# Kernel optimization log

Measured on AMD Instinct MI355X. Metric: run time of the kernel, lower is better.

## Reference

```python
import jax, jax.numpy as jnp
import numpy as np

N, E, H, DE = 50000, 800000, 128, 16

def silu(x):
    return x * jax.nn.sigmoid(x)

def setup_inputs() -> dict:
    key = jax.random.key(0)
    ks = jax.random.split(key, 24)
    def W(k, i, o, s=0.02):
        return (jax.random.normal(k, (i, o), jnp.float32) * s)
    inp = {
        'h': jax.random.normal(ks[0], (N, H), jnp.float32),
        'coord': jax.random.normal(ks[1], (N, 3), jnp.float32),
        'edge_index': jax.random.randint(ks[2], (2, E), 0, N),
        'edge_attr': jax.random.normal(ks[3], (E, DE), jnp.float32),
        # mes_mlp: Linear(2H+1+DE -> H), SiLU, Linear(H -> H), SiLU
        'mes_w1': W(ks[4], 2 * H + 1 + DE, H), 'mes_b1': jnp.zeros((H,), jnp.float32),
        'mes_w2': W(ks[5], H, H),              'mes_b2': jnp.zeros((H,), jnp.float32),
        # edge_mlp: Linear(H+1+DE -> H), SiLU, Linear(H -> H)
        'edge_w1': W(ks[6], H + 1 + DE, H),    'edge_b1': jnp.zeros((H,), jnp.float32),
        'edge_w2': W(ks[7], H, H),             'edge_b2': jnp.zeros((H,), jnp.float32),
        # node_mlp: Linear(H+H -> H), SiLU, Linear(H -> H)
        'node_w1': W(ks[8], 2 * H, H),         'node_b1': jnp.zeros((H,), jnp.float32),
        'node_w2': W(ks[9], H, H),             'node_b2': jnp.zeros((H,), jnp.float32),
        # coord_mlp: Linear(H -> H), SiLU, Linear(H -> 1, no bias, xavier gain 0.001)
        'coord_w1': W(ks[10], H, H),           'coord_b1': jnp.zeros((H,), jnp.float32),
        'coord_w2': W(ks[11], H, 1, s=0.001),
    }
    return inp

def reference(h, coord, edge_index, edge_attr,
              mes_w1, mes_b1, mes_w2, mes_b2,
              edge_w1, edge_b1, edge_w2, edge_b2,
              node_w1, node_b1, node_w2, node_b2,
              coord_w1, coord_b1, coord_w2):
    row, col = edge_index[0], edge_index[1]
    n = h.shape[0]
    # coord2radial
    coord_diff = coord[row] - coord[col]                        # [E,3]
    radial = jnp.sum(coord_diff ** 2, axis=1, keepdims=True)    # [E,1]
    norm = jnp.sqrt(radial + 1e-8)
    coord_diff = coord_diff / (norm + 1.0)
    # mes_model
    mes_in = jnp.concatenate([h[row], h[col], radial, edge_attr], axis=1)
    edge_feat = silu(silu(mes_in @ mes_w1 + mes_b1) @ mes_w2 + mes_b2)  # [E,H]
    # coord_model (agg='sum', no tanh)
    trans = coord_diff * (silu(edge_feat @ coord_w1 + coord_b1) @ coord_w2)  # [E,3]
    coord = coord + jax.ops.segment_sum(trans, col, num_segments=n)
    # node_model (recurrent)
    agg = jax.ops.segment_sum(edge_feat, col, num_segments=n)   # [N,H]
    node_in = jnp.concatenate([h, agg], axis=1)
    h = h + (silu(node_in @ node_w1 + node_b1) @ node_w2 + node_b2)
    # edge_model
    edge_in = jnp.concatenate([edge_feat, radial, edge_attr], axis=1)
    edge_out = silu(edge_in @ edge_w1 + edge_b1) @ edge_w2 + edge_b2
    return (h, coord, edge_out)
```

## Files before the change

kernel.cpp:

```cpp
#include <hip/hip_runtime.h>
#include <cstdint>
#include <cstddef>

typedef float f32x4 __attribute__((ext_vector_type(4)));
typedef __bf16 bf16x8 __attribute__((ext_vector_type(8)));
typedef __bf16 bf16x4 __attribute__((ext_vector_type(4)));
typedef unsigned short u16;

#define Hdim 128
#define DEdim 16
#define TP 40

__device__ __forceinline__ float bf2f(uint32_t lo16){
  return __builtin_bit_cast(float, lo16 << 16);
}
__device__ __forceinline__ float bfhi(uint32_t v){
  return __builtin_bit_cast(float, v & 0xffff0000u);
}
__device__ __forceinline__ float silu_f(float x){
  return x * __builtin_amdgcn_rcpf(1.0f + __expf(-x));
}
__device__ __forceinline__ uint2 pack4(f32x4 v){
  bf16x4 p;
  #pragma unroll
  for (int i=0;i<4;++i) p[i] = (__bf16)v[i];
  return __builtin_bit_cast(uint2, p);
}
__device__ __forceinline__ uint2 silu_pack4(const f32x4& v, f32x4* sout=nullptr){
  f32x4 s;
  #pragma unroll
  for (int i=0;i<4;++i) s[i] = silu_f(v[i]);
  if (sout) *sout = s;
  return pack4(s);
}

template<int KC>
__device__ __forceinline__ void gemm_sw(
    const u16* A, int apitch,
    const u16* __restrict__ Wt, int kpad, int woff,
    int wv, int cidx, int hi, f32x4 (&acc)[4][2])
{
  const u16* w0p = Wt + (size_t)((wv*2+0)*16 + cidx)*kpad + woff + hi*8;
  const u16* w1p = Wt + (size_t)((wv*2+1)*16 + cidx)*kpad + woff + hi*8;
  const u16* ap  = A + (size_t)cidx*apitch + hi*8;
  #pragma unroll
  for (int kc=0; kc<KC; ++kc){
    bf16x8 w0 = *(const bf16x8*)(w0p + kc*32);
    bf16x8 w1 = *(const bf16x8*)(w1p + kc*32);
    #pragma unroll
    for (int et=0; et<4; ++et){
      bf16x8 a = *(const bf16x8*)(ap + et*16*apitch + kc*32);
      acc[et][0] = __builtin_amdgcn_mfma_f32_16x16x32_bf16(w0, a, acc[et][0], 0,0,0);
      acc[et][1] = __builtin_amdgcn_mfma_f32_16x16x32_bf16(w1, a, acc[et][1], 0,0,0);
    }
  }
}

__device__ __forceinline__ void acc_bias(const float* __restrict__ bias,
                                         int wv, int hi, f32x4 (&acc)[4][2])
{
  f32x4 b0 = *(const f32x4*)(bias + (wv*2+0)*16 + hi*4);
  f32x4 b1 = *(const f32x4*)(bias + (wv*2+1)*16 + hi*4);
  #pragma unroll
  for (int et=0;et<4;++et){ acc[et][0]=b0; acc[et][1]=b1; }
}

template<int SP>
__device__ __forceinline__ void write_silu_S(u16* S, f32x4 (&acc)[4][2],
                                             int wv, int cidx, int hi)
{
  #pragma unroll
  for (int et=0; et<4; ++et){
    const int e = et*16 + cidx;
    #pragma unroll
    for (int j=0;j<2;++j){
      const int f0 = (wv*2+j)*16 + hi*4;
      *(uint2*)(S + (size_t)e*SP + f0) = silu_pack4(acc[et][j]);
    }
  }
}

template<bool PROJ, bool GATHER>
__global__ __launch_bounds__(256, PROJ?4:3) void egcl_edge(
    const float* __restrict__ h, const float* __restrict__ coord,
    const int* __restrict__ ei, const float* __restrict__ ea,
    const u16* __restrict__ projf, const int* __restrict__ pos,
    const float* __restrict__ mes_b1, const float* __restrict__ mes_b2,
    const float* __restrict__ edge_b1, const float* __restrict__ edge_b2,
    const float* __restrict__ coord_b1, const float* __restrict__ coord_w2,
    const u16* __restrict__ w_mes1t, const u16* __restrict__ w_mes2t,
    const u16* __restrict__ w_coord1t, const u16* __restrict__ w_edge1t,
    const u16* __restrict__ w_edge2t,
    float* __restrict__ agg, u16* __restrict__ featb,
    float* __restrict__ out_coord, float* __restrict__ out_edge, int E)
{
  constexpr int SP = PROJ ? 136 : 264;
  __shared__ u16 S[64*SP];
  __shared__ u16 T[64*TP];
  __shared__ float cds[64*4];
  __shared__ float tvs[4][64];
  __shared__ int cnode[64];

  const int tid  = threadIdx.x;
  const int lane = tid & 63;
  const int wv   = tid >> 6;
  const int e0   = blockIdx.x * 64;
  const int cidx = lane & 15;
  const int hi   = lane >> 4;

  ushort4 gr[4][2], gc[4][2];
  if constexpr (PROJ){
    #pragma unroll
    for (int et=0;et<4;++et){
      int eg = e0 + et*16 + cidx; if (eg >= E) eg = E-1;
      const int rn = ei[eg], cn = ei[E + eg];
      const u16* pr = projf + (size_t)rn*256 + wv*32 + hi*4;
      const u16* pc = projf + (size_t)cn*256 + 128 + wv*32 + hi*4;
      gr[et][0] = *(const ushort4*)(pr);
      gr[et][1] = *(const ushort4*)(pr + 16);
      gc[et][0] = *(const ushort4*)(pc);
      gc[et][1] = *(const ushort4*)(pc + 16);
    }
  }

  {
    const int le   = wv*16 + (lane>>2);
    const int part = lane & 3;
    int eg = e0 + le; if (eg >= E) eg = E-1;
    if constexpr (!PROJ){
      const int rn = ei[eg], cn = ei[E + eg];
      const float* src = ((part<2) ? h + (size_t)rn*Hdim : h + (size_t)cn*Hdim) + (part&1)*64;
      u16* dst = S + (size_t)le*SP + part*64;
      #pragma unroll
      for (int q=0;q<16;++q){
        float4 v = ((const float4*)src)[q];
        bf16x4 o = {(__bf16)v.x,(__bf16)v.y,(__bf16)v.z,(__bf16)v.w};
        *(bf16x4*)(dst + q*4) = o;
      }
    }
    if (part == 0){
      const int rn = ei[eg], cn = ei[E + eg];
      cnode[le] = cn;
      const float dx = coord[(size_t)rn*3+0] - coord[(size_t)cn*3+0];
      const float dy = coord[(size_t)rn*3+1] - coord[(size_t)cn*3+1];
      const float dz = coord[(size_t)rn*3+2] - coord[(size_t)cn*3+2];
      const float radial = dx*dx + dy*dy + dz*dz;
      const float inv = __builtin_amdgcn_rcpf(sqrtf(radial + 1e-8f) + 1.0f);
      cds[le*4+0]=dx*inv; cds[le*4+1]=dy*inv; cds[le*4+2]=dz*inv; cds[le*4+3]=radial;
      u16* tp = T + le*TP;
      const float4* eap = (const float4*)(ea + (size_t)eg*DEdim);
      #pragma unroll
      for (int q=0;q<4;++q){
        float4 v = eap[q];
        bf16x4 o = {(__bf16)v.x,(__bf16)v.y,(__bf16)v.z,(__bf16)v.w};
        *(bf16x4*)(tp + q*4) = o;
      }
      bf16x4 z = {(__bf16)0.f,(__bf16)0.f,(__bf16)0.f,(__bf16)0.f};
      *(bf16x4*)(tp+16) = z; *(bf16x4*)(tp+20) = z;
      *(bf16x4*)(tp+24) = z; *(bf16x4*)(tp+28) = z;
      *(__bf16*)(tp+16) = (__bf16)radial;
    }
  }
  __syncthreads();

  f32x4 acc[4][2];

  acc_bias(mes_b1, wv, hi, acc);
  if constexpr (PROJ){
    #pragma unroll
    for (int et=0;et<4;++et){
      #pragma unroll
      for (int j=0;j<2;++j){
        acc[et][j][0] += bf2f(gr[et][j].x) + bf2f(gc[et][j].x);
        acc[et][j][1] += bf2f(gr[et][j].y) + bf2f(gc[et][j].y);
        acc[et][j][2] += bf2f(gr[et][j].z) + bf2f(gc[et][j].z);
        acc[et][j][3] += bf2f(gr[et][j].w) + bf2f(gc[et][j].w);
      }
    }
    gemm_sw<1>(T, TP, w_mes1t, 288, 256, wv, cidx, hi, acc);
  } else {
    gemm_sw<8>(S, SP, w_mes1t, 288, 0,   wv, cidx, hi, acc);
    gemm_sw<1>(T, TP, w_mes1t, 288, 256, wv, cidx, hi, acc);
    __syncthreads();
  }
  write_silu_S<SP>(S, acc, wv, cidx, hi);
  __syncthreads();

  acc_bias(mes_b2, wv, hi, acc);
  gemm_sw<4>(S, SP, w_mes2t, 128, 0, wv, cidx, hi, acc);
  uint2 ps[4][2];
  #pragma unroll
  for (int et=0;et<4;++et)
    #pragma unroll
    for (int j=0;j<2;++j){
      f32x4 sv;
      ps[et][j] = silu_pack4(acc[et][j], &sv);
      if constexpr (!GATHER){
        const int e = et*16 + cidx;
        if (e0 + e < E){
          const int f0 = (wv*2+j)*16 + hi*4;
          #pragma unroll
          for (int i=0;i<4;++i)
            atomicAdd(agg + (size_t)cnode[e]*Hdim + f0 + i, sv[i]);
        }
      }
    }
  __syncthreads();
  #pragma unroll
  for (int et=0;et<4;++et)
    #pragma unroll
    for (int j=0;j<2;++j)
      *(uint2*)(S + (size_t)(et*16+cidx)*SP + (wv*2+j)*16 + hi*4) = ps[et][j];
  __syncthreads();

  if constexpr (GATHER){
    const int row = tid >> 2, seg = tid & 3;
    if (e0 + row < E){
      const int4* s = (const int4*)(S + (size_t)row*SP + seg*32);
      int4* d = (int4*)(featb + (size_t)pos[e0+row]*Hdim + seg*32);
      d[0]=s[0]; d[1]=s[1]; d[2]=s[2]; d[3]=s[3];
    }
  }

  acc_bias(coord_b1, wv, hi, acc);
  gemm_sw<4>(S, SP, w_coord1t, 128, 0, wv, cidx, hi, acc);
  {
    f32x4 cw0 = *(const f32x4*)(coord_w2 + (wv*2+0)*16 + hi*4);
    f32x4 cw1 = *(const f32x4*)(coord_w2 + (wv*2+1)*16 + hi*4);
    #pragma unroll
    for (int et=0;et<4;++et){
      float p = 0.f;
      #pragma unroll
      for (int i=0;i<4;++i)
        p += silu_f(acc[et][0][i])*cw0[i] + silu_f(acc[et][1][i])*cw1[i];
      p += __shfl_xor(p, 16);
      p += __shfl_xor(p, 32);
      if (hi == 0) tvs[wv][et*16+cidx] = p;
    }
  }

  acc_bias(edge_b1, wv, hi, acc);
  gemm_sw<4>(S, SP, w_edge1t, 160, 0,   wv, cidx, hi, acc);
  gemm_sw<1>(T, TP, w_edge1t, 160, 128, wv, cidx, hi, acc);
  #pragma unroll
  for (int et=0;et<4;++et)
    #pragma unroll
    for (int j=0;j<2;++j)
      ps[et][j] = silu_pack4(acc[et][j]);
  __syncthreads();
  #pragma unroll
  for (int et=0;et<4;++et)
    #pragma unroll
    for (int j=0;j<2;++j)
      *(uint2*)(S + (size_t)(et*16+cidx)*SP + (wv*2+j)*16 + hi*4) = ps[et][j];
  __syncthreads();

  acc_bias(edge_b2, wv, hi, acc);
  gemm_sw<4>(S, SP, w_edge2t, 128, 0, wv, cidx, hi, acc);
  #pragma unroll
  for (int et=0;et<4;++et){
    const int e = e0 + et*16 + cidx;
    if (e < E){
      #pragma unroll
      for (int j=0;j<2;++j)
        *(f32x4*)(out_edge + (size_t)e*Hdim + (wv*2+j)*16 + hi*4) = acc[et][j];
    }
  }

  if (tid < 192){
    const int le = tid/3, d = tid - le*3;
    if (e0 + le < E){
      const float t4 = tvs[0][le]+tvs[1][le]+tvs[2][le]+tvs[3][le];
      atomicAdd(out_coord + (size_t)cnode[le]*3 + d, cds[le*4+d]*t4);
    }
  }
}

__global__ __launch_bounds__(256, 4) void egcl_proj(
    const float* __restrict__ h, const u16* __restrict__ w_mes1t,
    u16* __restrict__ proj, int N)
{
  __shared__ u16 S[64*136];
  const int tid=threadIdx.x, lane=tid&63, wv=tid>>6, cidx=lane&15, hi=lane>>4;
  const int r0 = blockIdx.x*64, half = blockIdx.y;
  {
    const int le = tid>>2, part = tid&3;
    int g = r0 + le; if (g >= N) g = N-1;
    const float* src = h + (size_t)g*Hdim + part*32;
    u16* dst = S + (size_t)le*136 + part*32;
    #pragma unroll
    for (int q=0;q<8;++q){
      float4 v = ((const float4*)src)[q];
      bf16x4 o = {(__bf16)v.x,(__bf16)v.y,(__bf16)v.z,(__bf16)v.w};
      *(bf16x4*)(dst + q*4) = o;
    }
  }
  __syncthreads();
  f32x4 acc[4][2];
  #pragma unroll
  for (int et=0;et<4;++et){ acc[et][0]=(f32x4){0,0,0,0}; acc[et][1]=(f32x4){0,0,0,0}; }
  gemm_sw<4>(S, 136, w_mes1t, 288, half*128, wv, cidx, hi, acc);
  #pragma unroll
  for (int et=0;et<4;++et){
    const int g = r0 + et*16 + cidx;
    if (g < N){
      #pragma unroll
      for (int j=0;j<2;++j)
        *(uint2*)(proj + (size_t)g*256 + half*128 + (wv*2+j)*16 + hi*4) = pack4(acc[et][j]);
    }
  }
}

template<bool GATHER>
__global__ __launch_bounds__(256, 4) void egcl_node(
    const float* __restrict__ h, const float* __restrict__ agg,
    const int* __restrict__ offs, const int* __restrict__ deg,
    const u16* __restrict__ featb,
    const float* __restrict__ node_b1, const float* __restrict__ node_b2,
    const u16* __restrict__ w_node1t, const u16* __restrict__ w_node2t,
    float* __restrict__ out_h, int N)
{
  __shared__ u16 Ab[64*264];
  const int tid=threadIdx.x, lane=tid&63, wv=tid>>6, cidx=lane&15, hi=lane>>4;
  const int r0 = blockIdx.x*64;
  {
    const int le = tid>>2, part = tid&3;
    int g = r0 + le; if (g >= N) g = N-1;
    const float* src = h + (size_t)g*Hdim + part*32;
    u16* dst = Ab + (size_t)le*264 + part*32;
    #pragma unroll
    for (int q=0;q<8;++q){
      float4 v = ((const float4*)src)[q];
      bf16x4 o = {(__bf16)v.x,(__bf16)v.y,(__bf16)v.z,(__bf16)v.w};
      *(bf16x4*)(dst + q*4) = o;
    }
  }
  if constexpr (GATHER){
    const int le = tid>>2, part = tid&3;
    const int g = r0 + le;
    float a[32];
    #pragma unroll
    for (int q=0;q<32;++q) a[q]=0.f;
    if (g < N){
      const int s = offs[g], dg = deg[g];
      const u16* base = featb + (size_t)s*Hdim + part*32;
      #pragma unroll 2
      for (int r=0;r<dg;++r){
        const uint4* rp = (const uint4*)(base + (size_t)r*Hdim);
        #pragma unroll
        for (int q=0;q<4;++q){
          uint4 w = rp[q];
          a[q*8+0] += bf2f(w.x & 0xffffu); a[q*8+1] += bfhi(w.x);
          a[q*8+2] += bf2f(w.y & 0xffffu); a[q*8+3] += bfhi(w.y);
          a[q*8+4] += bf2f(w.z & 0xffffu); a[q*8+5] += bfhi(w.z);
          a[q*8+6] += bf2f(w.w & 0xffffu); a[q*8+7] += bfhi(w.w);
        }
      }
    }
    u16* dst = Ab + (size_t)le*264 + 128 + part*32;
    #pragma unroll
    for (int q=0;q<8;++q){
      bf16x4 o = {(__bf16)a[q*4+0],(__bf16)a[q*4+1],(__bf16)a[q*4+2],(__bf16)a[q*4+3]};
      *(bf16x4*)(dst + q*4) = o;
    }
  } else {
    const int le = tid>>2, part = tid&3;
    int g = r0 + le; if (g >= N) g = N-1;
    const float* src = agg + (size_t)g*Hdim + part*32;
    u16* dst = Ab + (size_t)le*264 + 128 + part*32;
    #pragma unroll
    for (int q=0;q<8;++q){
      float4 v = ((const float4*)src)[q];
      bf16x4 o = {(__bf16)v.x,(__bf16)v.y,(__bf16)v.z,(__bf16)v.w};
      *(bf16x4*)(dst + q*4) = o;
    }
  }
  __syncthreads();

  f32x4 acc[4][2];
  acc_bias(node_b1, wv, hi, acc);
  gemm_sw<8>(Ab, 264, w_node1t, 256, 0, wv, cidx, hi, acc);
  __syncthreads();
  write_silu_S<264>(Ab, acc, wv, cidx, hi);
  __syncthreads();
  acc_bias(node_b2, wv, hi, acc);
  gemm_sw<4>(Ab, 264, w_node2t, 128, 0, wv, cidx, hi, acc);
  #pragma unroll
  for (int et=0;et<4;++et){
    const int g = r0 + et*16 + cidx;
    if (g < N){
      #pragma unroll
      for (int j=0;j<2;++j){
        const int f0 = (wv*2+j)*16 + hi*4;
        f32x4 hv = *(const f32x4*)(h + (size_t)g*Hdim + f0);
        hv += acc[et][j];
        *(f32x4*)(out_h + (size_t)g*Hdim + f0) = hv;
      }
    }
  }
}

__global__ void egcl_init(const float* __restrict__ coord, float* __restrict__ out_coord,
                          int nc, float* __restrict__ zf, int nzf,
                          int* __restrict__ zi, int nzi)
{
  const int i = blockIdx.x*256 + threadIdx.x;
  if (i < nc) out_coord[i] = coord[i];
  if (zf && i < nzf) zf[i] = 0.f;
  if (zi && i < nzi) zi[i] = 0;
}

__global__ void egcl_wconv7(
    const float* s0, const float* s1, const float* s2, const float* s3,
    const float* s4, const float* s5, const float* s6, u16* __restrict__ dst)
{
  static const int kpads[7]  = {288,128,128,160,128,256,128};
  static const int Ks[7]     = {273,128,128,145,128,256,128};
  static const int modes[7]  = {1,0,0,2,0,0,0};
  const int gi = blockIdx.x*256 + threadIdx.x;
  int w = 0, off = 0, boff = 0;
  #pragma unroll
  for (int t=0;t<7;++t){
    const int sz = 128*kpads[t];
    if (gi >= off && gi < off + sz){ w = t; boff = off; }
    off += sz;
  }
  if (gi >= off) return;
  const float* srcs[7] = {s0,s1,s2,s3,s4,s5,s6};
  const int li = gi - boff;
  const int kpad = kpads[w], K = Ks[w], mode = modes[w];
  const int c = li / kpad, k = li - c*kpad;
  int ks;
  if (mode==1)      ks = (k<256) ? k : (k<272 ? k+1 : (k==272 ? 256 : -1));
  else if (mode==2) ks = (k<128) ? k : (k<144 ? k+1 : (k==144 ? 128 : -1));
  else              ks = (k<K) ? k : -1;
  const float v = (ks>=0) ? srcs[w][(size_t)ks*128 + c] : 0.f;
  *(__bf16*)(dst + gi) = (__bf16)v;
}

__global__ void k_hist(const int* __restrict__ ei, int* __restrict__ hist, int E){
  const int i = blockIdx.x*256 + threadIdx.x;
  if (i < E) atomicAdd(&hist[ei[E + i]], 1);
}
__global__ void k_scan1(const int* __restrict__ hist, int* __restrict__ partial, int N){
  __shared__ int s[256];
  const int t = threadIdx.x, i = blockIdx.x*256 + t;
  s[t] = (i < N) ? hist[i] : 0;
  __syncthreads();
  for (int o=128; o>0; o>>=1){ if (t < o) s[t] += s[t+o]; __syncthreads(); }
  if (t == 0) partial[blockIdx.x] = s[0];
}
__global__ void k_scan2(int* __restrict__ partial, int G){
  if (blockIdx.x == 0 && threadIdx.x == 0){
    int run = 0;
    for (int i=0;i<G;++i){ const int v = partial[i]; partial[i] = run; run += v; }
  }
}
__global__ void k_scan3(const int* __restrict__ hist, const int* __restrict__ partial,
                        int* __restrict__ offs, int* __restrict__ cursor, int N){
  __shared__ int s[256];
  const int t = threadIdx.x, i = blockIdx.x*256 + t;
  const int v = (i < N) ? hist[i] : 0;
  s[t] = v;
  __syncthreads();
  for (int o=1; o<256; o<<=1){
    int x = (t >= o) ? s[t-o] : 0;
    __syncthreads();
    s[t] += x;
    __syncthreads();
  }
  const int ex = s[t] - v + partial[blockIdx.x];
  if (i < N){ offs[i] = ex; cursor[i] = ex; }
}
__global__ void k_scatter(const int* __restrict__ ei, int* __restrict__ cursor,
                          int* __restrict__ pos, int E){
  const int i = blockIdx.x*256 + threadIdx.x;
  if (i < E){
    const int c = ei[E + i];
    pos[i] = atomicAdd(&cursor[c], 1);
  }
}

extern "C" void kernel_launch(void* const* d_in, const int* in_sizes, int n_in,
                              void* d_out, int out_size, void* d_ws, size_t ws_size,
                              hipStream_t stream)
{
  const float* h       = (const float*)d_in[0];
  const float* coord   = (const float*)d_in[1];
  const int*   ei      = (const int*)d_in[2];
  const float* ea      = (const float*)d_in[3];
  const float* mes_w1  = (const float*)d_in[4];
  const float* mes_b1  = (const float*)d_in[5];
  const float* mes_w2  = (const float*)d_in[6];
  const float* mes_b2  = (const float*)d_in[7];
  const float* edge_w1 = (const float*)d_in[8];
  const float* edge_b1 = (const float*)d_in[9];
  const float* edge_w2 = (const float*)d_in[10];
  const float* edge_b2 = (const float*)d_in[11];
  const float* node_w1 = (const float*)d_in[12];
  const float* node_b1 = (const float*)d_in[13];
  const float* node_w2 = (const float*)d_in[14];
  const float* node_b2 = (const float*)d_in[15];
  const float* coord_w1= (const float*)d_in[16];
  const float* coord_b1= (const float*)d_in[17];
  const float* coord_w2= (const float*)d_in[18];

  const int N = in_sizes[0] / Hdim;
  const int E = in_sizes[2] / 2;
  const int G1 = (N + 255) / 256;

  char* ws = (char*)d_ws;
  const size_t wtot = (size_t)(288+128+128+160+128+256+128)*128;
  u16* wbase     = (u16*)ws;
  u16* w_mes1t   = wbase;
  u16* w_mes2t   = w_mes1t  + 128*288;
  u16* w_coord1t = w_mes2t  + 128*128;
  u16* w_edge1t  = w_coord1t+ 128*128;
  u16* w_edge2t  = w_edge1t + 128*160;
  u16* w_node1t  = w_edge2t + 128*128;
  u16* w_node2t  = w_node1t + 128*256;

  auto al = [](size_t x){ return (x + 255) & ~(size_t)255; };
  const size_t base   = al(wtot*2);
  const size_t o_feat = base;
  const size_t o_hist = o_feat + al((size_t)E*Hdim*2);
  const size_t o_offs = o_hist + al((size_t)N*4);
  const size_t o_cur  = o_offs + al((size_t)N*4);
  const size_t o_part = o_cur  + al((size_t)N*4);
  const size_t o_pos  = o_part + al((size_t)G1*4);
  const size_t gather_end = o_pos + al((size_t)E*4);
  const size_t o_proj = gather_end;
  const size_t proj_end = o_proj + (size_t)N*256*2;
  const bool gather = (ws_size >= gather_end);
  const bool proj   = (ws_size >= proj_end);

  float* out_h     = (float*)d_out;
  float* out_coord = out_h + (size_t)N*Hdim;
  float* out_edge  = out_coord + (size_t)N*3;

  const int wblocks = (int)((wtot + 255)/256);
  egcl_wconv7<<<wblocks, 256, 0, stream>>>(mes_w1, mes_w2, coord_w1, edge_w1,
                                           edge_w2, node_w1, node_w2, wbase);

  if (gather){
    u16* featb  = (u16*)(ws + o_feat);
    int* hist   = (int*)(ws + o_hist);
    int* offs   = (int*)(ws + o_offs);
    int* cursor = (int*)(ws + o_cur);
    int* partial= (int*)(ws + o_part);
    int* pos    = (int*)(ws + o_pos);
    u16* projp  = (u16*)(ws + o_proj);

    egcl_init<<<(N*3+255)/256, 256, 0, stream>>>(coord, out_coord, N*3, nullptr, 0, hist, N);
    k_hist<<<(E+255)/256, 256, 0, stream>>>(ei, hist, E);
    k_scan1<<<G1, 256, 0, stream>>>(hist, partial, N);
    k_scan2<<<1, 64, 0, stream>>>(partial, G1);
    k_scan3<<<G1, 256, 0, stream>>>(hist, partial, offs, cursor, N);
    k_scatter<<<(E+255)/256, 256, 0, stream>>>(ei, cursor, pos, E);

    if (proj){
      dim3 pg((N+63)/64, 2);
      egcl_proj<<<pg, 256, 0, stream>>>(h, w_mes1t, projp, N);
      egcl_edge<true,true><<<(E+63)/64, 256, 0, stream>>>(h, coord, ei, ea, projp, pos,
          mes_b1, mes_b2, edge_b1, edge_b2, coord_b1, coord_w2,
          w_mes1t, w_mes2t, w_coord1t, w_edge1t, w_edge2t,
          nullptr, featb, out_coord, out_edge, E);
    } else {
      egcl_edge<false,true><<<(E+63)/64, 256, 0, stream>>>(h, coord, ei, ea, nullptr, pos,
          mes_b1, mes_b2, edge_b1, edge_b2, coord_b1, coord_w2,
          w_mes1t, w_mes2t, w_coord1t, w_edge1t, w_edge2t,
          nullptr, featb, out_coord, out_edge, E);
    }
    egcl_node<true><<<(N+63)/64, 256, 0, stream>>>(h, nullptr, offs, hist, featb,
        node_b1, node_b2, w_node1t, w_node2t, out_h, N);
  } else {
    float* agg = (float*)(ws + base);
    egcl_init<<<(N*Hdim+255)/256, 256, 0, stream>>>(coord, out_coord, N*3, agg, N*Hdim, nullptr, 0);
    egcl_edge<false,false><<<(E+63)/64, 256, 0, stream>>>(h, coord, ei, ea, nullptr, nullptr,
        mes_b1, mes_b2, edge_b1, edge_b2, coord_b1, coord_w2,
        w_mes1t, w_mes2t, w_coord1t, w_edge1t, w_edge2t,
        agg, nullptr, out_coord, out_edge, E);
    egcl_node<false><<<(N+63)/64, 256, 0, stream>>>(h, agg, nullptr, nullptr, nullptr,
        node_b1, node_b2, w_node1t, w_node2t, out_h, N);
  }
}
```

Baseline: 636.6 us.

## Double-buffer edge-kernel shared tiles to drop barriers; parallelize partial scan

The projected edge-kernel path now uses two shared tiles (S1/S2) that ping-pong between MLP stages. This removes the extra barrier-plus-rewrite steps that used to copy packed activations back into a single buffer. Per-edge metadata (col index, normalized coord diff) is packed into the padding columns of those tiles, and the coord-MLP partial sums are combined with shared-memory atomics into a single array. The single-thread prefix scan over block partials becomes a 256-thread parallel scan when the block count fits, at the cost of slightly more shared memory per block.

```diff
diff --git a/kernel.cpp b/kernel.cpp
--- a/kernel.cpp
+++ b/kernel.cpp
@@ -94,13 +94,6 @@
     float* __restrict__ agg, u16* __restrict__ featb,
     float* __restrict__ out_coord, float* __restrict__ out_edge, int E)
 {
-  constexpr int SP = PROJ ? 136 : 264;
-  __shared__ u16 S[64*SP];
-  __shared__ u16 T[64*TP];
-  __shared__ float cds[64*4];
-  __shared__ float tvs[4][64];
-  __shared__ int cnode[64];
-
   const int tid  = threadIdx.x;
   const int lane = tid & 63;
   const int wv   = tid >> 6;
@@ -108,8 +101,14 @@
   const int cidx = lane & 15;
   const int hi   = lane >> 4;
 
-  ushort4 gr[4][2], gc[4][2];
   if constexpr (PROJ){
+    constexpr int SP = 136;
+    __shared__ u16 S1[64*SP];
+    __shared__ u16 S2[64*SP];
+    __shared__ u16 T[64*TP];
+    __shared__ float tvs[64];
+
+    ushort4 gr[4][2], gc[4][2];
     #pragma unroll
     for (int et=0;et<4;++et){
       int eg = e0 + et*16 + cidx; if (eg >= E) eg = E-1;
@@ -121,52 +120,41 @@
       gc[et][0] = *(const ushort4*)(pc);
       gc[et][1] = *(const ushort4*)(pc + 16);
     }
-  }
-
-  {
-    const int le   = wv*16 + (lane>>2);
-    const int part = lane & 3;
-    int eg = e0 + le; if (eg >= E) eg = E-1;
-    if constexpr (!PROJ){
-      const int rn = ei[eg], cn = ei[E + eg];
-      const float* src = ((part<2) ? h + (size_t)rn*Hdim : h + (size_t)cn*Hdim) + (part&1)*64;
-      u16* dst = S + (size_t)le*SP + part*64;
-      #pragma unroll
-      for (int q=0;q<16;++q){
-        float4 v = ((const float4*)src)[q];
-        bf16x4 o = {(__bf16)v.x,(__bf16)v.y,(__bf16)v.z,(__bf16)v.w};
-        *(bf16x4*)(dst + q*4) = o;
-      }
-    }
-    if (part == 0){
-      const int rn = ei[eg], cn = ei[E + eg];
-      cnode[le] = cn;
-      const float dx = coord[(size_t)rn*3+0] - coord[(size_t)cn*3+0];
-      const float dy = coord[(size_t)rn*3+1] - coord[(size_t)cn*3+1];
-      const float dz = coord[(size_t)rn*3+2] - coord[(size_t)cn*3+2];
-      const float radial = dx*dx + dy*dy + dz*dz;
-      const float inv = __builtin_amdgcn_rcpf(sqrtf(radial + 1e-8f) + 1.0f);
-      cds[le*4+0]=dx*inv; cds[le*4+1]=dy*inv; cds[le*4+2]=dz*inv; cds[le*4+3]=radial;
-      u16* tp = T + le*TP;
-      const float4* eap = (const float4*)(ea + (size_t)eg*DEdim);
-      #pragma unroll
-      for (int q=0;q<4;++q){
-        float4 v = eap[q];
-        bf16x4 o = {(__bf16)v.x,(__bf16)v.y,(__bf16)v.z,(__bf16)v.w};
-        *(bf16x4*)(tp + q*4) = o;
-      }
-      bf16x4 z = {(__bf16)0.f,(__bf16)0.f,(__bf16)0.f,(__bf16)0.f};
-      *(bf16x4*)(tp+16) = z; *(bf16x4*)(tp+20) = z;
-      *(bf16x4*)(tp+24) = z; *(bf16x4*)(tp+28) = z;
-      *(__bf16*)(tp+16) = (__bf16)radial;
-    }
-  }
-  __syncthreads();
-
-  f32x4 acc[4][2];
-
-  acc_bias(mes_b1, wv, hi, acc);
-  if constexpr (PROJ){
+
+    {
+      const int le   = wv*16 + (lane>>2);
+      const int part = lane & 3;
+      int eg = e0 + le; if (eg >= E) eg = E-1;
+      if (part == 0){
+        const int rn = ei[eg], cn = ei[E + eg];
+        *(int*)(S2 + (size_t)le*SP + 128) = cn;
+        const float dx = coord[(size_t)rn*3+0] - coord[(size_t)cn*3+0];
+        const float dy = coord[(size_t)rn*3+1] - coord[(size_t)cn*3+1];
+        const float dz = coord[(size_t)rn*3+2] - coord[(size_t)cn*3+2];
+        const float radial = dx*dx + dy*dy + dz*dz;
+        const float inv = __builtin_amdgcn_rcpf(sqrtf(radial + 1e-8f) + 1.0f);
+        float* cp = (float*)(S1 + (size_t)le*SP + 128);
+        cp[0]=dx*inv; cp[1]=dy*inv; cp[2]=dz*inv;
+        u16* tp = T + le*TP;
+        const float4* eap = (const float4*)(ea + (size_t)eg*DEdim);
+        #pragma unroll
+        for (int q=0;q<4;++q){
+          float4 v = eap[q];
+          bf16x4 o = {(__bf16)v.x,(__bf16)v.y,(__bf16)v.z,(__bf16)v.w};
+          *(bf16x4*)(tp + q*4) = o;
+        }
+        bf16x4 z = {(__bf16)0.f,(__bf16)0.f,(__bf16)0.f,(__bf16)0.f};
+        *(bf16x4*)(tp+16) = z; *(bf16x4*)(tp+20) = z;
+        *(bf16x4*)(tp+24) = z; *(bf16x4*)(tp+28) = z;
+        *(__bf16*)(tp+16) = (__bf16)radial;
+      }
+      if (tid < 64) tvs[tid] = 0.f;
+    }
+    __syncthreads();
+
+    f32x4 acc[4][2];
+
+    acc_bias(mes_b1, wv, hi, acc);
     #pragma unroll
     for (int et=0;et<4;++et){
       #pragma unroll
@@ -178,100 +166,223 @@
       }
     }
     gemm_sw<1>(T, TP, w_mes1t, 288, 256, wv, cidx, hi, acc);
+    write_silu_S<SP>(S1, acc, wv, cidx, hi);
+    __syncthreads();
+
+    acc_bias(mes_b2, wv, hi, acc);
+    gemm_sw<4>(S1, SP, w_mes2t, 128, 0, wv, cidx, hi, acc);
+    #pragma unroll
+    for (int et=0;et<4;++et)
+      #pragma unroll
+      for (int j=0;j<2;++j){
+        f32x4 sv;
+        uint2 pk = silu_pack4(acc[et][j], &sv);
+        *(uint2*)(S2 + (size_t)(et*16+cidx)*SP + (wv*2+j)*16 + hi*4) = pk;
+        if constexpr (!GATHER){
+          const int e = et*16 + cidx;
+          if (e0 + e < E){
+            const int cn = *(const int*)(S2 + (size_t)e*SP + 128);
+            const int f0 = (wv*2+j)*16 + hi*4;
+            #pragma unroll
+            for (int i=0;i<4;++i)
+              atomicAdd(agg + (size_t)cn*Hdim + f0 + i, sv[i]);
+          }
+        }
+      }
+    __syncthreads();
+
+    if constexpr (GATHER){
+      const int row = tid >> 2, seg = tid & 3;
+      if (e0 + row < E){
+        const int4* s = (const int4*)(S2 + (size_t)row*SP + seg*32);
+        int4* d = (int4*)(featb + (size_t)pos[e0+row]*Hdim + seg*32);
+        d[0]=s[0]; d[1]=s[1]; d[2]=s[2]; d[3]=s[3];
+      }
+    }
+
+    acc_bias(coord_b1, wv, hi, acc);
+    gemm_sw<4>(S2, SP, w_coord1t, 128, 0, wv, cidx, hi, acc);
+    {
+      f32x4 cw0 = *(const f32x4*)(coord_w2 + (wv*2+0)*16 + hi*4);
+      f32x4 cw1 = *(const f32x4*)(coord_w2 + (wv*2+1)*16 + hi*4);
+      #pragma unroll
+      for (int et=0;et<4;++et){
+        float p = 0.f;
+        #pragma unroll
+        for (int i=0;i<4;++i)
+          p += silu_f(acc[et][0][i])*cw0[i] + silu_f(acc[et][1][i])*cw1[i];
+        p += __shfl_xor(p, 16);
+        p += __shfl_xor(p, 32);
+        if (hi == 0) atomicAdd(&tvs[et*16+cidx], p);
+      }
+    }
+
+    acc_bias(edge_b1, wv, hi, acc);
+    gemm_sw<4>(S2, SP, w_edge1t, 160, 0,   wv, cidx, hi, acc);
+    gemm_sw<1>(T,  TP, w_edge1t, 160, 128, wv, cidx, hi, acc);
+    write_silu_S<SP>(S1, acc, wv, cidx, hi);
+    __syncthreads();
+
+    acc_bias(edge_b2, wv, hi, acc);
+    gemm_sw<4>(S1, SP, w_edge2t, 128, 0, wv, cidx, hi, acc);
+    #pragma unroll
+    for (int et=0;et<4;++et){
+      const int e = e0 + et*16 + cidx;
+      if (e < E){
+        #pragma unroll
+        for (int j=0;j<2;++j)
+          *(f32x4*)(out_edge + (size_t)e*Hdim + (wv*2+j)*16 + hi*4) = acc[et][j];
+      }
+    }
+
+    if (tid < 192){
+      const int le = tid/3, d = tid - le*3;
+      if (e0 + le < E){
+        const float* cp = (const float*)(S1 + (size_t)le*SP + 128);
+        const int cn = *(const int*)(S2 + (size_t)le*SP + 128);
+        atomicAdd(out_coord + (size_t)cn*3 + d, cp[d]*tvs[le]);
+      }
+    }
   } else {
+    constexpr int SP = 264;
+    __shared__ u16 S[64*SP];
+    __shared__ u16 T[64*TP];
+    __shared__ float cds[64*4];
+    __shared__ float tvs4[4][64];
+    __shared__ int cnode[64];
+
+    {
+      const int le   = wv*16 + (lane>>2);
+      const int part = lane & 3;
+      int eg = e0 + le; if (eg >= E) eg = E-1;
+      const int rn = ei[eg], cn = ei[E + eg];
+      const float* src = ((part<2) ? h + (size_t)rn*Hdim : h + (size_t)cn*Hdim) + (part&1)*64;
+      u16* dst = S + (size_t)le*SP + part*64;
+      #pragma unroll
+      for (int q=0;q<16;++q){
+        float4 v = ((const float4*)src)[q];
+        bf16x4 o = {(__bf16)v.x,(__bf16)v.y,(__bf16)v.z,(__bf16)v.w};
+        *(bf16x4*)(dst + q*4) = o;
+      }
+      if (part == 0){
+        cnode[le] = cn;
+        const float dx = coord[(size_t)rn*3+0] - coord[(size_t)cn*3+0];
+        const float dy = coord[(size_t)rn*3+1] - coord[(size_t)cn*3+1];
+        const float dz = coord[(size_t)rn*3+2] - coord[(size_t)cn*3+2];
+        const float radial = dx*dx + dy*dy + dz*dz;
+        const float inv = __builtin_amdgcn_rcpf(sqrtf(radial + 1e-8f) + 1.0f);
+        cds[le*4+0]=dx*inv; cds[le*4+1]=dy*inv; cds[le*4+2]=dz*inv; cds[le*4+3]=radial;
+        u16* tp = T + le*TP;
+        const float4* eap = (const float4*)(ea + (size_t)eg*DEdim);
+        #pragma unroll
+        for (int q=0;q<4;++q){
+          float4 v = eap[q];
+          bf16x4 o = {(__bf16)v.x,(__bf16)v.y,(__bf16)v.z,(__bf16)v.w};
+          *(bf16x4*)(tp + q*4) = o;
+        }
+        bf16x4 z = {(__bf16)0.f,(__bf16)0.f,(__bf16)0.f,(__bf16)0.f};
+        *(bf16x4*)(tp+16) = z; *(bf16x4*)(tp+20) = z;
+        *(bf16x4*)(tp+24) = z; *(bf16x4*)(tp+28) = z;
+        *(__bf16*)(tp+16) = (__bf16)radial;
+      }
+      ((float*)tvs4)[tid] = 0.f;
+    }
+    __syncthreads();
+
+    f32x4 acc[4][2];
+    acc_bias(mes_b1, wv, hi, acc);
     gemm_sw<8>(S, SP, w_mes1t, 288, 0,   wv, cidx, hi, acc);
     gemm_sw<1>(T, TP, w_mes1t, 288, 256, wv, cidx, hi, acc);
     __syncthreads();
-  }
-  write_silu_S<SP>(S, acc, wv, cidx, hi);
-  __syncthreads();
-
-  acc_bias(mes_b2, wv, hi, acc);
-  gemm_sw<4>(S, SP, w_mes2t, 128, 0, wv, cidx, hi, acc);
-  uint2 ps[4][2];
-  #pragma unroll
-  for (int et=0;et<4;++et)
-    #pragma unroll
-    for (int j=0;j<2;++j){
-      f32x4 sv;
-      ps[et][j] = silu_pack4(acc[et][j], &sv);
-      if constexpr (!GATHER){
-        const int e = et*16 + cidx;
-        if (e0 + e < E){
-          const int f0 = (wv*2+j)*16 + hi*4;
-          #pragma unroll
-          for (int i=0;i<4;++i)
-            atomicAdd(agg + (size_t)cnode[e]*Hdim + f0 + i, sv[i]);
+    write_silu_S<SP>(S, acc, wv, cidx, hi);
+    __syncthreads();
+
+    acc_bias(mes_b2, wv, hi, acc);
+    gemm_sw<4>(S, SP, w_mes2t, 128, 0, wv, cidx, hi, acc);
+    uint2 ps[4][2];
+    #pragma unroll
+    for (int et=0;et<4;++et)
+      #pragma unroll
+      for (int j=0;j<2;++j){
+        f32x4 sv;
+        ps[et][j] = silu_pack4(acc[et][j], &sv);
+        if constexpr (!GATHER){
+          const int e = et*16 + cidx;
+          if (e0 + e < E){
+            const int f0 = (wv*2+j)*16 + hi*4;
+            #pragma unroll
+            for (int i=0;i<4;++i)
+              atomicAdd(agg + (size_t)cnode[e]*Hdim + f0 + i, sv[i]);
+          }
         }
       }
-    }
-  __syncthreads();
-  #pragma unroll
-  for (int et=0;et<4;++et)
-    #pragma unroll
-    for (int j=0;j<2;++j)
-      *(uint2*)(S + (size_t)(et*16+cidx)*SP + (wv*2+j)*16 + hi*4) = ps[et][j];
-  __syncthreads();
-
-  if constexpr (GATHER){
-    const int row = tid >> 2, seg = tid & 3;
-    if (e0 + row < E){
-      const int4* s = (const int4*)(S + (size_t)row*SP + seg*32);
-      int4* d = (int4*)(featb + (size_t)pos[e0+row]*Hdim + seg*32);
-      d[0]=s[0]; d[1]=s[1]; d[2]=s[2]; d[3]=s[3];
-    }
-  }
-
-  acc_bias(coord_b1, wv, hi, acc);
-  gemm_sw<4>(S, SP, w_coord1t, 128, 0, wv, cidx, hi, acc);
-  {
-    f32x4 cw0 = *(const f32x4*)(coord_w2 + (wv*2+0)*16 + hi*4);
-    f32x4 cw1 = *(const f32x4*)(coord_w2 + (wv*2+1)*16 + hi*4);
+    __syncthreads();
+    #pragma unroll
+    for (int et=0;et<4;++et)
+      #pragma unroll
+      for (int j=0;j<2;++j)
+        *(uint2*)(S + (size_t)(et*16+cidx)*SP + (wv*2+j)*16 + hi*4) = ps[et][j];
+    __syncthreads();
+
+    if constexpr (GATHER){
+      const int row = tid >> 2, seg = tid & 3;
+      if (e0 + row < E){
+        const int4* s = (const int4*)(S + (size_t)row*SP + seg*32);
+        int4* d = (int4*)(featb + (size_t)pos[e0+row]*Hdim + seg*32);
+        d[0]=s[0]; d[1]=s[1]; d[2]=s[2]; d[3]=s[3];
+      }
+    }
+
+    acc_bias(coord_b1, wv, hi, acc);
+    gemm_sw<4>(S, SP, w_coord1t, 128, 0, wv, cidx, hi, acc);
+    {
+      f32x4 cw0 = *(const f32x4*)(coord_w2 + (wv*2+0)*16 + hi*4);
+      f32x4 cw1 = *(const f32x4*)(coord_w2 + (wv*2+1)*16 + hi*4);
+      #pragma unroll
+      for (int et=0;et<4;++et){
+        float p = 0.f;
+        #pragma unroll
+        for (int i=0;i<4;++i)
+          p += silu_f(acc[et][0][i])*cw0[i] + silu_f(acc[et][1][i])*cw1[i];
+        p += __shfl_xor(p, 16);
+        p += __shfl_xor(p, 32);
+        if (hi == 0) tvs4[wv][et*16+cidx] = p;
+      }
+    }
+
+    acc_bias(edge_b1, wv, hi, acc);
+    gemm_sw<4>(S, SP, w_edge1t, 160, 0,   wv, cidx, hi, acc);
+    gemm_sw<1>(T, TP, w_edge1t, 160, 128, wv, cidx, hi, acc);
+    #pragma unroll
+    for (int et=0;et<4;++et)
+      #pragma unroll
+      for (int j=0;j<2;++j)
+        ps[et][j] = silu_pack4(acc[et][j]);
+    __syncthreads();
+    #pragma unroll
+    for (int et=0;et<4;++et)
+      #pragma unroll
+      for (int j=0;j<2;++j)
+        *(uint2*)(S + (size_t)(et*16+cidx)*SP + (wv*2+j)*16 + hi*4) = ps[et][j];
+    __syncthreads();
+
+    acc_bias(edge_b2, wv, hi, acc);
+    gemm_sw<4>(S, SP, w_edge2t, 128, 0, wv, cidx, hi, acc);
     #pragma unroll
     for (int et=0;et<4;++et){
-      float p = 0.f;
-      #pragma unroll
-      for (int i=0;i<4;++i)
-        p += silu_f(acc[et][0][i])*cw0[i] + silu_f(acc[et][1][i])*cw1[i];
-      p += __shfl_xor(p, 16);
-      p += __shfl_xor(p, 32);
-      if (hi == 0) tvs[wv][et*16+cidx] = p;
-    }
-  }
-
-  acc_bias(edge_b1, wv, hi, acc);
-  gemm_sw<4>(S, SP, w_edge1t, 160, 0,   wv, cidx, hi, acc);
-  gemm_sw<1>(T, TP, w_edge1t, 160, 128, wv, cidx, hi, acc);
-  #pragma unroll
-  for (int et=0;et<4;++et)
-    #pragma unroll
-    for (int j=0;j<2;++j)
-      ps[et][j] = silu_pack4(acc[et][j]);
-  __syncthreads();
-  #pragma unroll
-  for (int et=0;et<4;++et)
-    #pragma unroll
-    for (int j=0;j<2;++j)
-      *(uint2*)(S + (size_t)(et*16+cidx)*SP + (wv*2+j)*16 + hi*4) = ps[et][j];
-  __syncthreads();
-
-  acc_bias(edge_b2, wv, hi, acc);
-  gemm_sw<4>(S, SP, w_edge2t, 128, 0, wv, cidx, hi, acc);
-  #pragma unroll
-  for (int et=0;et<4;++et){
-    const int e = e0 + et*16 + cidx;
-    if (e < E){
-      #pragma unroll
-      for (int j=0;j<2;++j)
-        *(f32x4*)(out_edge + (size_t)e*Hdim + (wv*2+j)*16 + hi*4) = acc[et][j];
-    }
-  }
-
-  if (tid < 192){
-    const int le = tid/3, d = tid - le*3;
-    if (e0 + le < E){
-      const float t4 = tvs[0][le]+tvs[1][le]+tvs[2][le]+tvs[3][le];
-      atomicAdd(out_coord + (size_t)cnode[le]*3 + d, cds[le*4+d]*t4);
+      const int e = e0 + et*16 + cidx;
+      if (e < E){
+        #pragma unroll
+        for (int j=0;j<2;++j)
+          *(f32x4*)(out_edge + (size_t)e*Hdim + (wv*2+j)*16 + hi*4) = acc[et][j];
+      }
+    }
+    if (tid < 192){
+      const int le = tid/3, d = tid - le*3;
+      if (e0 + le < E){
+        const float t4 = tvs4[0][le]+tvs4[1][le]+tvs4[2][le]+tvs4[3][le];
+        atomicAdd(out_coord + (size_t)cnode[le]*3 + d, cds[le*4+d]*t4);
+      }
     }
   }
 }
@@ -451,7 +562,20 @@
   if (t == 0) partial[blockIdx.x] = s[0];
 }
 __global__ void k_scan2(int* __restrict__ partial, int G){
-  if (blockIdx.x == 0 && threadIdx.x == 0){
+  __shared__ int s[256];
+  const int t = threadIdx.x;
+  if (G <= 256){
+    const int v = (t < G) ? partial[t] : 0;
+    s[t] = v;
+    __syncthreads();
+    for (int o=1; o<256; o<<=1){
+      int x = (t >= o) ? s[t-o] : 0;
+      __syncthreads();
+      s[t] += x;
+      __syncthreads();
+    }
+    if (t < G) partial[t] = s[t] - v;
+  } else if (t == 0){
     int run = 0;
     for (int i=0;i<G;++i){ const int v = partial[i]; partial[i] = run; run += v; }
   }
@@ -554,7 +678,7 @@
     egcl_init<<<(N*3+255)/256, 256, 0, stream>>>(coord, out_coord, N*3, nullptr, 0, hist, N);
     k_hist<<<(E+255)/256, 256, 0, stream>>>(ei, hist, E);
     k_scan1<<<G1, 256, 0, stream>>>(hist, partial, N);
-    k_scan2<<<1, 64, 0, stream>>>(partial, G1);
+    k_scan2<<<1, 256, 0, stream>>>(partial, G1);
     k_scan3<<<G1, 256, 0, stream>>>(hist, partial, offs, cursor, N);
     k_scatter<<<(E+255)/256, 256, 0, stream>>>(ei, cursor, pos, E);
 
```

New measurement: 658.8 us. 1.03x slower.
